# Kernel optimization log

Hardware: AMD Instinct MI355X
Metric: run time of the kernel (lower is better)

## Reference

```python
import jax, jax.numpy as jnp
import numpy as np

B, C, HH, WW, HEADS = 4, 64, 256, 256, 8
CH = C // HEADS              # 8 per-head dim
HID = int(C * 2.66)          # 170
EPS_LN = 1e-5
EPS = 1e-6
QK_NORM = 1.0
# crpe windows for 8 heads: {3:2, 5:3, 7:3}; each conv input split = head_split*Ch*2
WINDOWS = [(3, 2), (5, 3), (7, 3)]


def conv2d(x, w, b=None, groups=1, pad=0):
    out = jax.lax.conv_general_dilated(
        x, w, (1, 1), [(pad, pad), (pad, pad)],
        dimension_numbers=('NCHW', 'OIHW', 'NCHW'), feature_group_count=groups)
    return out if b is None else out + b[None, :, None, None]


def setup_inputs() -> dict:
    key = jax.random.key(0)
    ks = jax.random.split(key, 32)
    p = lambda k, shp, s=0.05: jax.random.normal(k, shp, jnp.float32) * s
    inp = {
        'x': jax.random.normal(ks[0], (B, HH * WW, C), jnp.float32),
        'ln1_w': jnp.ones((C,), jnp.float32) + p(ks[1], (C,), 0.01),
        'sca_w': p(ks[2], (C, C, 1, 1)), 'sca_b': p(ks[3], (C,)),
        'dw1_w': p(ks[4], (2 * C, C, 1, 1)),          # 1x1 dim->2dim
        'dw2_w': p(ks[5], (C, 2, 3, 3)),              # grouped 3x3, groups=C, in/grp=2
        'qkv_w': p(ks[6], (3 * C, C, 1, 1)),
        'qkv_dw_w': p(ks[7], (3 * C, 1, 3, 3)),       # depthwise 3x3
        'temperature': jnp.ones((HEADS, 1, 1), jnp.float32),
        'r3_w': p(ks[8], (2, 2 * CH, 3, 3)), 'r3_b': p(ks[9], (2,)),
        'r5_w': p(ks[10], (3, 2 * CH, 5, 5)), 'r5_b': p(ks[11], (3,)),
        'r7_w': p(ks[12], (3, 2 * CH, 7, 7)), 'r7_b': p(ks[13], (3,)),
        'proj_w': p(ks[14], (C, C, 1, 1)),
        'ln2_w': jnp.ones((C,), jnp.float32) + p(ks[15], (C,), 0.01),
        'pin_w': p(ks[16], (2 * HID, C, 1, 1)),
        'ffn_dw_w': p(ks[17], (2 * HID, 1, 3, 3)),
        'pout_w': p(ks[18], (C, HID, 1, 1)),
        'H': HH, 'W': WW,
    }
    return inp


def biasfree_ln(x, w):
    # BiasFree LayerNorm over channel dim of NCHW (var only, no mean-subtract)
    sigma = jnp.var(x, axis=1, keepdims=True)
    return x / jnp.sqrt(sigma + EPS_LN) * w[None, :, None, None]


def refine_att(q, k, H, W, convs):
    # q: (B,h,N,Ch)  k: (B,h,Ch,N) -> per-head conv relative position map (B,h,N,1)
    b, h, N, Ch = q.shape
    q_img = q.transpose(0, 1, 3, 2).reshape(b, h, Ch, H, W)
    k_img = k.reshape(b, h, Ch, H, W)
    qk = jnp.concatenate([q_img, k_img], axis=2).reshape(b, h * 2 * Ch, H, W)
    splits = np.cumsum([s * 2 * Ch for _, s in WINDOWS])[:-1]
    parts = jnp.split(qk, splits, axis=1)
    outs = [conv2d(xp, wt, bs, groups=g, pad=win // 2)
            for (win, g), (wt, bs), xp in zip(WINDOWS, convs, parts)]
    att = jnp.concatenate(outs, axis=1)           # (b, h, H, W)
    return att.reshape(b, h, 1, H * W).transpose(0, 1, 3, 2)  # (b,h,N,1)


def attention(x, sca_w, sca_b, dw1_w, dw2_w, qkv_w, qkv_dw_w, temperature,
              refine_convs, proj_w, H, W):
    b, c, _, _ = x.shape
    N = H * W
    xsca = conv2d(jnp.mean(x, axis=(2, 3), keepdims=True), sca_w, sca_b)
    x1 = conv2d(conv2d(x, dw1_w), dw2_w, groups=c, pad=1)
    qkv = conv2d(conv2d(x, qkv_w), qkv_dw_w, groups=3 * c, pad=1)
    q, k, v = jnp.split(qkv, 3, axis=1)
    q = q.reshape(b, HEADS, CH, N).transpose(0, 1, 3, 2)  # b h N Ch
    k = k.reshape(b, HEADS, CH, N)                        # b h Ch N
    v = v.reshape(b, HEADS, CH, N).transpose(0, 1, 3, 2)  # b h N Ch
    q = q / (jnp.linalg.norm(q, axis=-1, keepdims=True) / QK_NORM + EPS)
    k = k / (jnp.linalg.norm(k, axis=-2, keepdims=True) / QK_NORM + EPS)
    refine_w = jax.nn.sigmoid(refine_att(q, k, H, W, refine_convs))
    attn = k @ v                                           # b h Ch Ch
    out_num = jnp.sum(v, axis=-2, keepdims=True) + q @ attn
    ksum = jnp.sum(k, axis=-1, keepdims=True)              # b h Ch 1
    out_den = jnp.asarray(N, q.dtype) + q @ ksum + EPS     # b h N 1 (bcast to Ch)
    out = out_num / out_den * temperature
    out = out * refine_w
    out = out.transpose(0, 1, 3, 2).reshape(b, c, H, W)
    out = out * xsca * jax.nn.gelu(x1, approximate=False)
    return conv2d(out, proj_w)


def feedforward(x, pin_w, ffn_dw_w, pout_w):
    h = conv2d(x, pin_w)
    h = conv2d(h, ffn_dw_w, groups=2 * HID, pad=1)
    h1, h2 = jnp.split(h, 2, axis=1)
    return conv2d(jax.nn.gelu(h1, approximate=False) * h2, pout_w)


def reference(x, ln1_w, sca_w, sca_b, dw1_w, dw2_w, qkv_w, qkv_dw_w, temperature,
              r3_w, r3_b, r5_w, r5_b, r7_w, r7_b, proj_w, ln2_w,
              pin_w, ffn_dw_w, pout_w, H, W):
    b = x.shape[0]
    xi = x.reshape(b, H, W, C).transpose(0, 3, 1, 2)  # NCHW
    refine_convs = [(r3_w, r3_b), (r5_w, r5_b), (r7_w, r7_b)]
    xi = xi + attention(biasfree_ln(xi, ln1_w), sca_w, sca_b, dw1_w, dw2_w,
                        qkv_w, qkv_dw_w, temperature, refine_convs, proj_w, H, W)
    xi = xi + feedforward(biasfree_ln(xi, ln2_w), pin_w, ffn_dw_w, pout_w)
    return xi
```

## Files before the change

kernel.cpp:

```cpp
#include <hip/hip_runtime.h>
#include <math.h>
#include <stdio.h>

#define BB 4
#define NP 65536

typedef unsigned short u16;
typedef unsigned int u32;
typedef __attribute__((ext_vector_type(8))) short short8;
typedef __attribute__((ext_vector_type(4))) float f32x4;

__device__ __forceinline__ float bf2f(u16 u) { return __uint_as_float((u32)u << 16); }
__device__ __forceinline__ u16 f2bf(float f) {
  u32 u = __float_as_uint(f);
  u = (u + 0x7FFFu + ((u >> 16) & 1u)) >> 16;
  return (u16)u;
}
__device__ __forceinline__ float gelu_f(float x) {
  return 0.5f * x * (1.f + erff(x * 0.70710678118654752f));
}

__global__ __launch_bounds__(256) void k_trans_stats(const float* __restrict__ x,
                                                     float* __restrict__ xi,
                                                     u16* __restrict__ xb1,
                                                     float* __restrict__ meanraw) {
  __shared__ float tile[64 * 65];
  __shared__ float s1a[64], s2a[64], sig[64], cm[64];
  int b = blockIdx.y;
  long n0 = (long)blockIdx.x * 64;
  int t = threadIdx.x;
  for (int i = t; i < 4096; i += 256) {
    int nl = i >> 6, c = i & 63;
    tile[nl * 65 + c] = x[((long)b * NP + n0 + nl) * 64 + c];
  }
  if (t < 64) { s1a[t] = 0.f; s2a[t] = 0.f; cm[t] = 0.f; }
  __syncthreads();
  {
    int nl = t & 63, part = t >> 6;
    float p1 = 0.f, p2 = 0.f;
    for (int cc = 0; cc < 16; cc++) {
      float v = tile[nl * 65 + part * 16 + cc];
      p1 += v; p2 += v * v;
    }
    atomicAdd(&s1a[nl], p1); atomicAdd(&s2a[nl], p2);
  }
  __syncthreads();
  if (t < 64) {
    float m = s1a[t] * (1.f / 64.f);
    float var = s2a[t] * (1.f / 64.f) - m * m;
    sig[t] = rsqrtf(var + 1e-5f);
  }
  __syncthreads();
  int nl = t & 63;
  int part = t >> 6;
  float sgv = sig[nl];
  for (int j = 0; j < 16; j++) {
    int i = t + 256 * j;
    int c = i >> 6;
    float v = tile[nl * 65 + c];
    xi[((long)b * 64 + c) * NP + n0 + nl] = v;
    float a = v * sgv;
    for (int off = 32; off; off >>= 1) a += __shfl_down(a, off);
    if ((t & 63) == 0) atomicAdd(&cm[c], a);
  }
  {
    u16* rp = xb1 + ((long)b * NP + n0 + nl) * 64 + part * 16;
    uint4 pk[2];
    u32 tmp[8];
#pragma unroll
    for (int g = 0; g < 2; g++) {
#pragma unroll
      for (int e = 0; e < 4; e++) {
        float v0 = tile[nl * 65 + part * 16 + g * 8 + 2 * e] * sgv;
        float v1 = tile[nl * 65 + part * 16 + g * 8 + 2 * e + 1] * sgv;
        tmp[e] = (u32)f2bf(v0) | ((u32)f2bf(v1) << 16);
      }
      pk[g].x = tmp[0]; pk[g].y = tmp[1]; pk[g].z = tmp[2]; pk[g].w = tmp[3];
      *(uint4*)(rp + g * 8) = pk[g];
    }
  }
  __syncthreads();
  if (t < 64) atomicAdd(&meanraw[b * 64 + t], cm[t]);
}

__global__ void k_xsca(const float* __restrict__ meanraw, const float* __restrict__ lnw,
                       const float* __restrict__ sca_w, const float* __restrict__ sca_b,
                       float* __restrict__ xsca) {
  int t = threadIdx.x;
  int b = t >> 6, co = t & 63;
  float a = sca_b[co];
  for (int ci = 0; ci < 64; ci++)
    a += sca_w[co * 64 + ci] * meanraw[b * 64 + ci] * lnw[ci] * (1.f / 65536.f);
  xsca[t] = a;
}

__global__ void k_foldW1b(const float* __restrict__ qkv_w, const float* __restrict__ dw1_w,
                          const float* __restrict__ lnw, u16* __restrict__ W1b) {
  int i = blockIdx.x * 256 + threadIdx.x;
  if (i < 320 * 64) {
    int co = i >> 6, ci = i & 63;
    float w = (co < 192) ? qkv_w[co * 64 + ci] : dw1_w[(co - 192) * 64 + ci];
    W1b[i] = f2bf(w * lnw[ci]);
  }
}
__global__ void k_foldW2b(const float* __restrict__ pin_w, const float* __restrict__ lnw,
                          u16* __restrict__ W2b) {
  int i = blockIdx.x * 256 + threadIdx.x;
  if (i < 384 * 64) {
    int co = i >> 6, ci = i & 63;
    float v = 0.f;
    if (co < 340) {
      int pair = co >> 1, which = co & 1;
      v = pin_w[(pair + which * 170) * 64 + ci] * lnw[ci];
    }
    W2b[i] = f2bf(v);
  }
}
__global__ void k_foldWpb(const float* __restrict__ w, u16* __restrict__ Wpb) {
  int i = blockIdx.x * 256 + threadIdx.x;
  if (i < 4096) Wpb[i] = f2bf(w[i]);
}
__global__ void k_tpout(const float* __restrict__ w, float* __restrict__ WoT) {
  int i = blockIdx.x * 256 + threadIdx.x;
  if (i < 170 * 64) { int ci = i >> 6, co = i & 63; WoT[ci * 64 + co] = w[co * 170 + ci]; }
}

template <int EPI>
__global__ __launch_bounds__(256) void k_mgemm(const u16* __restrict__ in, long in_bs,
                                               const u16* __restrict__ W,
                                               u16* __restrict__ outp, long out_bs,
                                               float* __restrict__ xo,
                                               u16* __restrict__ xb2r) {
  int t = threadIdx.x;
  int lane = t & 63, wv = t >> 6;
  int l15 = lane & 15, quad = lane >> 4;
  int pxw = blockIdx.x * 256 + wv * 64;
  int co0 = blockIdx.y * 64;
  int b = blockIdx.z;
  const u16* inb = in + (long)b * in_bs;

  short8 aw[4][2];
#pragma unroll
  for (int t4 = 0; t4 < 4; t4++)
#pragma unroll
    for (int kf = 0; kf < 2; kf++)
      aw[t4][kf] = *(const short8*)(W + (long)(co0 + t4 * 16 + l15) * 64 + kf * 32 + quad * 8);

  f32x4 acc[4][4];
#pragma unroll
  for (int t4 = 0; t4 < 4; t4++)
#pragma unroll
    for (int p = 0; p < 4; p++) acc[t4][p] = (f32x4){0.f, 0.f, 0.f, 0.f};

#pragma unroll
  for (int p = 0; p < 4; p++) {
    long px = pxw + p * 16 + l15;
    short8 bf0 = *(const short8*)(inb + px * 64 + quad * 8);
    short8 bf1 = *(const short8*)(inb + px * 64 + 32 + quad * 8);
#pragma unroll
    for (int t4 = 0; t4 < 4; t4++) {
      acc[t4][p] = __builtin_amdgcn_mfma_f32_16x16x32_bf16(aw[t4][0], bf0, acc[t4][p], 0, 0, 0);
      acc[t4][p] = __builtin_amdgcn_mfma_f32_16x16x32_bf16(aw[t4][1], bf1, acc[t4][p], 0, 0, 0);
    }
  }

  if (EPI == 0) {
    u16* ob = outp + (long)b * out_bs;
#pragma unroll
    for (int t4 = 0; t4 < 4; t4++)
#pragma unroll
      for (int p = 0; p < 4; p++) {
#pragma unroll
        for (int reg = 0; reg < 4; reg++) {
          int co = co0 + t4 * 16 + quad * 4 + reg;
          ob[(long)co * NP + pxw + p * 16 + l15] = f2bf(acc[t4][p][reg]);
        }
      }
  } else {
#pragma unroll
    for (int p = 0; p < 4; p++) {
      long px = pxw + p * 16 + l15;
      float xv[16];
      float s1 = 0.f, s2 = 0.f;
#pragma unroll
      for (int t4 = 0; t4 < 4; t4++)
#pragma unroll
        for (int reg = 0; reg < 4; reg++) {
          int co = t4 * 16 + quad * 4 + reg;
          float v = xo[((long)b * 64 + co) * NP + px] + acc[t4][p][reg];
          xv[t4 * 4 + reg] = v;
          s1 += v; s2 += v * v;
        }
      s1 += __shfl_xor(s1, 16); s2 += __shfl_xor(s2, 16);
      s1 += __shfl_xor(s1, 32); s2 += __shfl_xor(s2, 32);
      float m = s1 * (1.f / 64.f);
      float var = s2 * (1.f / 64.f) - m * m;
      float sg = rsqrtf(var + 1e-5f);
#pragma unroll
      for (int t4 = 0; t4 < 4; t4++)
#pragma unroll
        for (int reg = 0; reg < 4; reg++) {
          int co = t4 * 16 + quad * 4 + reg;
          xo[((long)b * 64 + co) * NP + px] = xv[t4 * 4 + reg];
        }
      u16* rp = xb2r + ((long)b * NP + px) * 64;
#pragma unroll
      for (int t4 = 0; t4 < 4; t4++) {
        u32 u0 = (u32)f2bf(xv[t4 * 4 + 0] * sg) | ((u32)f2bf(xv[t4 * 4 + 1] * sg) << 16);
        u32 u1 = (u32)f2bf(xv[t4 * 4 + 2] * sg) | ((u32)f2bf(xv[t4 * 4 + 3] * sg) << 16);
        uint2 pk; pk.x = u0; pk.y = u1;
        *(uint2*)(rp + t4 * 16 + quad * 4) = pk;
      }
    }
  }
}

__device__ __forceinline__ void dw4(const u16* __restrict__ img, int y, int x0, int lane,
                                    const float* __restrict__ w9, float d[4]) {
  d[0] = 0.f; d[1] = 0.f; d[2] = 0.f; d[3] = 0.f;
#pragma unroll
  for (int dy = -1; dy <= 1; dy++) {
    int r = y + dy;
    float v1, v2, v3, v4;
    if ((unsigned)r < 256u) {
      ushort4 u = *(const ushort4*)(img + r * 256 + x0);
      v1 = bf2f(u.x); v2 = bf2f(u.y); v3 = bf2f(u.z); v4 = bf2f(u.w);
    } else { v1 = 0.f; v2 = 0.f; v3 = 0.f; v4 = 0.f; }
    float v0 = __shfl_up(v4, 1);  if (lane == 0)  v0 = 0.f;
    float v5 = __shfl_down(v1, 1); if (lane == 63) v5 = 0.f;
    float w0 = w9[(dy + 1) * 3], w1 = w9[(dy + 1) * 3 + 1], w2 = w9[(dy + 1) * 3 + 2];
    d[0] += w0 * v0 + w1 * v1 + w2 * v2;
    d[1] += w0 * v1 + w1 * v2 + w2 * v3;
    d[2] += w0 * v2 + w1 * v3 + w2 * v4;
    d[3] += w0 * v3 + w1 * v4 + w2 * v5;
  }
}

__global__ __launch_bounds__(256) void k_dwqkv(const u16* __restrict__ P,
                                               const float* __restrict__ dww,
                                               u16* __restrict__ Qn, u16* __restrict__ Kn,
                                               u16* __restrict__ Vn) {
  int t = threadIdx.x;
  int lane = t & 63, wv = t >> 6;
  int by = blockIdx.y;
  int ph = by >> 3, h = by & 7;
  int b = blockIdx.z;
  int y = blockIdx.x * 4 + wv;
  int x0 = lane * 4;
  long n = (long)y * 256 + x0;
  int cbase = ph * 64 + h * 8;
  const u16* Pb = P + ((long)b * 192 + cbase) * NP;
  const float* wb = dww + cbase * 9;

  float v[8][4];
#pragma unroll
  for (int c = 0; c < 8; c++)
    dw4(Pb + (long)c * NP, y, x0, lane, wb + c * 9, v[c]);

  if (ph < 2) {
    float s2[4] = {0.f, 0.f, 0.f, 0.f};
#pragma unroll
    for (int c = 0; c < 8; c++)
#pragma unroll
      for (int j = 0; j < 4; j++) s2[j] += v[c][j] * v[c][j];
#pragma unroll
    for (int j = 0; j < 4; j++) s2[j] = 1.f / (sqrtf(s2[j]) + 1e-6f);
#pragma unroll
    for (int c = 0; c < 8; c++)
#pragma unroll
      for (int j = 0; j < 4; j++) v[c][j] *= s2[j];
  }
  u16* dst = (ph == 0) ? Qn : (ph == 1) ? Kn : Vn;
#pragma unroll
  for (int c = 0; c < 8; c++) {
    ushort4 st;
    st.x = f2bf(v[c][0]); st.y = f2bf(v[c][1]);
    st.z = f2bf(v[c][2]); st.w = f2bf(v[c][3]);
    *(ushort4*)(dst + ((long)b * 64 + h * 8 + c) * NP + n) = st;
  }
}

__global__ __launch_bounds__(256) void k_stats(const u16* __restrict__ Kn,
                                               const u16* __restrict__ Vn,
                                               float* __restrict__ stats) {
  int t = threadIdx.x;
  int lane = t & 63;
  int h = blockIdx.y, b = blockIdx.z;
  long px = (long)blockIdx.x * 1024 + t * 4;
  const u16* Kb = Kn + ((long)b * 64 + h * 8) * NP + px;
  const u16* Vb = Vn + ((long)b * 64 + h * 8) * NP + px;
  float kf[8][4], vf[8][4];
#pragma unroll
  for (int c = 0; c < 8; c++) {
    ushort4 ku = *(const ushort4*)(Kb + (long)c * NP);
    kf[c][0] = bf2f(ku.x); kf[c][1] = bf2f(ku.y);
    kf[c][2] = bf2f(ku.z); kf[c][3] = bf2f(ku.w);
  }
#pragma unroll
  for (int c = 0; c < 8; c++) {
    ushort4 vu = *(const ushort4*)(Vb + (long)c * NP);
    vf[c][0] = bf2f(vu.x); vf[c][1] = bf2f(vu.y);
    vf[c][2] = bf2f(vu.z); vf[c][3] = bf2f(vu.w);
  }
  __shared__ float sred[80];
  if (t < 80) sred[t] = 0.f;
  __syncthreads();
#pragma unroll
  for (int i = 0; i < 8; i++) {
#pragma unroll
    for (int j = 0; j < 8; j++) {
      float a = kf[i][0] * vf[j][0] + kf[i][1] * vf[j][1] +
                kf[i][2] * vf[j][2] + kf[i][3] * vf[j][3];
      a += __shfl_xor(a, 1); a += __shfl_xor(a, 2); a += __shfl_xor(a, 4);
      a += __shfl_xor(a, 8); a += __shfl_xor(a, 16); a += __shfl_xor(a, 32);
      if (lane == ((i * 8 + j) & 63)) atomicAdd(&sred[i * 8 + j], a);
    }
    {
      float a = kf[i][0] + kf[i][1] + kf[i][2] + kf[i][3];
      a += __shfl_xor(a, 1); a += __shfl_xor(a, 2); a += __shfl_xor(a, 4);
      a += __shfl_xor(a, 8); a += __shfl_xor(a, 16); a += __shfl_xor(a, 32);
      if (lane == ((64 + i) & 63)) atomicAdd(&sred[64 + i], a);
    }
    {
      float a = vf[i][0] + vf[i][1] + vf[i][2] + vf[i][3];
      a += __shfl_xor(a, 1); a += __shfl_xor(a, 2); a += __shfl_xor(a, 4);
      a += __shfl_xor(a, 8); a += __shfl_xor(a, 16); a += __shfl_xor(a, 32);
      if (lane == ((72 + i) & 63)) atomicAdd(&sred[72 + i], a);
    }
  }
  __syncthreads();
  if (t < 80) atomicAdd(&stats[((long)b * 8 + h) * 80 + t], sred[t]);
}

__global__ __launch_bounds__(256) void k_dwg(const u16* __restrict__ P,
                                             const float* __restrict__ dw2_w,
                                             u16* __restrict__ G) {
  int t = threadIdx.x;
  int lane = t & 63, wv = t >> 6;
  int c = blockIdx.y, b = blockIdx.z;
  int y = blockIdx.x * 4 + wv;
  int x0 = lane * 4;
  long n = (long)y * 256 + x0;
  const u16* Pb = P + (long)b * 128 * NP;
  float d1[4], d2[4];
  dw4(Pb + (long)(2 * c) * NP, y, x0, lane, dw2_w + c * 18, d1);
  dw4(Pb + (long)(2 * c + 1) * NP, y, x0, lane, dw2_w + c * 18 + 9, d2);
  ushort4 st;
  st.x = f2bf(gelu_f(d1[0] + d2[0])); st.y = f2bf(gelu_f(d1[1] + d2[1]));
  st.z = f2bf(gelu_f(d1[2] + d2[2])); st.w = f2bf(gelu_f(d1[3] + d2[3]));
  *(ushort4*)(G + ((long)b * 64 + c) * NP + n) = st;
}

__global__ __launch_bounds__(256) void k_dwgate(const u16* __restrict__ P,
                                                const float* __restrict__ dww,
                                                u16* __restrict__ Hb) {
  int t = threadIdx.x;
  int lane = t & 63, wv = t >> 6;
  int c = blockIdx.y, b = blockIdx.z;
  int y = blockIdx.x * 4 + wv;
  int x0 = lane * 4;
  long n = (long)y * 256 + x0;
  const u16* Pb = P + (long)b * 384 * NP;
  float d1[4], d2[4];
  dw4(Pb + (long)(2 * c) * NP, y, x0, lane, dww + c * 9, d1);
  dw4(Pb + (long)(2 * c + 1) * NP, y, x0, lane, dww + (170 + c) * 9, d2);
  ushort4 st;
  st.x = f2bf(gelu_f(d1[0]) * d2[0]); st.y = f2bf(gelu_f(d1[1]) * d2[1]);
  st.z = f2bf(gelu_f(d1[2]) * d2[2]); st.w = f2bf(gelu_f(d1[3]) * d2[3]);
  *(ushort4*)(Hb + ((long)b * 170 + c) * NP + n) = st;
}

__device__ __forceinline__ float bfe_elem(uint2 v, int e) {
  u32 w = (e < 2) ? v.x : v.y;
  return bf2f((e & 1) ? (u16)(w >> 16) : (u16)w);
}

template <int WIN>
__device__ __forceinline__ void dwacc(const u16* __restrict__ img, int y, int x0, int lane,
                                      const float* __restrict__ w, float a[4]) {
  const int R = WIN / 2;
#pragma unroll
  for (int dy = -R; dy <= R; dy++) {
    int r = y + dy;
    uint2 q; q.x = 0u; q.y = 0u;
    if ((unsigned)r < 256u) q = *(const uint2*)(img + r * 256 + x0);
    uint2 ql, qr;
    ql.x = (u32)__shfl_up((int)q.x, 1);  ql.y = (u32)__shfl_up((int)q.y, 1);
    qr.x = (u32)__shfl_down((int)q.x, 1); qr.y = (u32)__shfl_down((int)q.y, 1);
    if (lane == 0)  { ql.x = 0u; ql.y = 0u; }
    if (lane == 63) { qr.x = 0u; qr.y = 0u; }
    float f[4 + 2 * R];
#pragma unroll
    for (int i = 0; i < R; i++) f[i] = bfe_elem(ql, 4 - R + i);
    f[R + 0] = bf2f((u16)q.x); f[R + 1] = bf2f((u16)(q.x >> 16));
    f[R + 2] = bf2f((u16)q.y); f[R + 3] = bf2f((u16)(q.y >> 16));
#pragma unroll
    for (int i = 0; i < R; i++) f[R + 4 + i] = bfe_elem(qr, i);
    const float* wr = w + (dy + R) * WIN;
#pragma unroll
    for (int dx = 0; dx < WIN; dx++) {
      float wv = wr[dx];
      a[0] += wv * f[dx];     a[1] += wv * f[dx + 1];
      a[2] += wv * f[dx + 2]; a[3] += wv * f[dx + 3];
    }
  }
}

template <int WIN>
__device__ void refine_body(const u16* __restrict__ Qh, const u16* __restrict__ Kh,
                            const float* __restrict__ wp, float bias,
                            float* __restrict__ ro, int y, int x0, int lane) {
  float a[4] = {bias, bias, bias, bias};
#pragma unroll
  for (int ph = 0; ph < 2; ph++) {
    const u16* src = ph ? Kh : Qh;
#pragma unroll 2
    for (int ch = 0; ch < 8; ch++)
      dwacc<WIN>(src + (long)ch * NP, y, x0, lane, wp + (ph * 8 + ch) * WIN * WIN, a);
  }
  float4 o;
  o.x = 1.f / (1.f + expf(-a[0])); o.y = 1.f / (1.f + expf(-a[1]));
  o.z = 1.f / (1.f + expf(-a[2])); o.w = 1.f / (1.f + expf(-a[3]));
  *(float4*)(ro + (long)y * 256 + x0) = o;
}

__global__ __launch_bounds__(256) void k_refine(
    const u16* __restrict__ Qn, const u16* __restrict__ Kn,
    const float* __restrict__ r3w, const float* __restrict__ r3b,
    const float* __restrict__ r5w, const float* __restrict__ r5b,
    const float* __restrict__ r7w, const float* __restrict__ r7b,
    float* __restrict__ refW) {
  int t = threadIdx.x, lane = t & 63, wv = t >> 6;
  int h = (blockIdx.y + 5) & 7;
  int b = blockIdx.z;
  int y = blockIdx.x * 4 + wv, x0 = lane * 4;
  const u16* Qh = Qn + ((long)b * 64 + h * 8) * NP;
  const u16* Kh = Kn + ((long)b * 64 + h * 8) * NP;
  float* ro = refW + ((long)(b * 8 + h)) * NP;
  if (h < 2)      refine_body<3>(Qh, Kh, r3w + h * 16 * 9, r3b[h], ro, y, x0, lane);
  else if (h < 5) refine_body<5>(Qh, Kh, r5w + (h - 2) * 16 * 25, r5b[h - 2], ro, y, x0, lane);
  else            refine_body<7>(Qh, Kh, r7w + (h - 5) * 16 * 49, r7b[h - 5], ro, y, x0, lane);
}

__global__ __launch_bounds__(256) void k_attn(
    const u16* __restrict__ Qn, const float* __restrict__ stats,
    const float* __restrict__ refw, const float* __restrict__ temp,
    const float* __restrict__ xsca, const u16* __restrict__ G,
    u16* __restrict__ Orows) {
  int b = blockIdx.y;
  int t = threadIdx.x;
  __shared__ float s[640];
  __shared__ float sx[64];
  for (int i = t; i < 640; i += 256) s[i] = stats[(long)b * 640 + i];
  if (t < 64) sx[t] = xsca[b * 64 + t];
  __syncthreads();
  long n = (long)blockIdx.x * 256 + t;
  u16* rp = Orows + ((long)b * NP + n) * 64;
#pragma unroll
  for (int h = 0; h < 8; h++) {
    const float* sh = s + h * 80;
    float q[8];
#pragma unroll
    for (int i = 0; i < 8; i++) q[i] = bf2f(Qn[((long)b * 64 + h * 8 + i) * NP + n]);
    float den = 65536.f + 1e-6f;
#pragma unroll
    for (int i = 0; i < 8; i++) den += q[i] * sh[64 + i];
    float tr = temp[h] * refw[((long)b * 8 + h) * NP + n] / den;
    u32 pk[4];
#pragma unroll
    for (int j2 = 0; j2 < 4; j2++) {
      float o01[2];
#pragma unroll
      for (int e = 0; e < 2; e++) {
        int j = j2 * 2 + e;
        float num = sh[72 + j];
#pragma unroll
        for (int i = 0; i < 8; i++) num += q[i] * sh[i * 8 + j];
        int ci = h * 8 + j;
        o01[e] = num * tr * sx[ci] * bf2f(G[((long)b * 64 + ci) * NP + n]);
      }
      pk[j2] = (u32)f2bf(o01[0]) | ((u32)f2bf(o01[1]) << 16);
    }
    uint4 v; v.x = pk[0]; v.y = pk[1]; v.z = pk[2]; v.w = pk[3];
    *(uint4*)(rp + h * 8) = v;
  }
}

__global__ __launch_bounds__(256) void k_pout(const u16* __restrict__ Hb,
                                              const float* __restrict__ WoT,
                                              float* __restrict__ xo) {
  int n = blockIdx.x * 256 + threadIdx.x;
  int b = blockIdx.z;
  const u16* ip = Hb + (long)b * 170 * NP + n;
  float acc[64];
#pragma unroll
  for (int j = 0; j < 64; j++) acc[j] = 0.f;
#pragma unroll 2
  for (int ci = 0; ci < 170; ci++) {
    float xv = bf2f(ip[(long)ci * NP]);
    const float* wr = WoT + ci * 64;
#pragma unroll
    for (int j = 0; j < 64; j++) acc[j] += wr[j] * xv;
  }
  float* xp = xo + (long)b * 64 * NP + n;
#pragma unroll
  for (int c = 0; c < 64; c++) xp[(long)c * NP] += acc[c];
}

extern "C" void kernel_launch(void* const* d_in, const int* in_sizes, int n_in,
                              void* d_out, int out_size, void* d_ws, size_t ws_size,
                              hipStream_t stream) {
  const float* x        = (const float*)d_in[0];
  const float* ln1_w    = (const float*)d_in[1];
  const float* sca_w    = (const float*)d_in[2];
  const float* sca_b    = (const float*)d_in[3];
  const float* dw1_w    = (const float*)d_in[4];
  const float* dw2_w    = (const float*)d_in[5];
  const float* qkv_w    = (const float*)d_in[6];
  const float* qkv_dw_w = (const float*)d_in[7];
  const float* temp     = (const float*)d_in[8];
  const float* r3w = (const float*)d_in[9],  *r3b = (const float*)d_in[10];
  const float* r5w = (const float*)d_in[11], *r5b = (const float*)d_in[12];
  const float* r7w = (const float*)d_in[13], *r7b = (const float*)d_in[14];
  const float* proj_w   = (const float*)d_in[15];
  const float* ln2_w    = (const float*)d_in[16];
  const float* pin_w    = (const float*)d_in[17];
  const float* ffn_dw_w = (const float*)d_in[18];
  const float* pout_w   = (const float*)d_in[19];
  float* out = (float*)d_out;
  char* wsb = (char*)d_ws;

  const size_t Mi = 1048576;
  u16* xb1   = (u16*)(wsb);
  u16* Qn    = (u16*)(wsb + 32 * Mi);
  u16* Kn    = (u16*)(wsb + 64 * Mi);
  u16* G     = (u16*)(wsb + 96 * Mi);
  u16* Preg  = (u16*)(wsb + 128 * Mi);
  float* refW    = (float*)(wsb + 224 * Mi);
  float* Fm      = (float*)(wsb + 232 * Mi);
  float* stats   = Fm;
  float* meanraw = Fm + 2560;
  float* xscab   = Fm + 2816;
  float* WoT     = Fm + 3072;
  u16* W1b = (u16*)(Fm + 13952);
  u16* W2b = W1b + 20480;
  u16* Wpb = W2b + 24576;
  u16* xb2 = xb1;
  u16* Orows = Kn;
  u16* Hb = Qn;
  u16* Vn = G;

  const size_t needed = 232 * Mi + 13952 * 4 + (20480 + 24576 + 4096) * 2;
  if (ws_size < needed) {
    fprintf(stderr, "kernel_launch: ws_size %zu < needed %zu\n", ws_size, needed);
    return;
  }

  hipMemsetAsync(stats, 0, (2560 + 256) * 4, stream);
  k_foldW1b<<<80, 256, 0, stream>>>(qkv_w, dw1_w, ln1_w, W1b);
  k_foldW2b<<<96, 256, 0, stream>>>(pin_w, ln2_w, W2b);
  k_foldWpb<<<16, 256, 0, stream>>>(proj_w, Wpb);
  k_tpout<<<43, 256, 0, stream>>>(pout_w, WoT);

  k_trans_stats<<<dim3(1024, BB), 256, 0, stream>>>(x, out, xb1, meanraw);
  k_xsca<<<1, 256, 0, stream>>>(meanraw, ln1_w, sca_w, sca_b, xscab);

  k_mgemm<0><<<dim3(256, 3, BB), 256, 0, stream>>>(xb1, (long)NP * 64, W1b,
                                                   Preg, 192L * NP, nullptr, nullptr);
  k_dwqkv<<<dim3(64, 24, BB), 256, 0, stream>>>(Preg, qkv_dw_w, Qn, Kn, Vn);
  k_stats<<<dim3(64, 8, BB), 256, 0, stream>>>(Kn, Vn, stats);

  k_mgemm<0><<<dim3(256, 2, BB), 256, 0, stream>>>(xb1, (long)NP * 64, W1b + 192 * 64,
                                                   Preg, 128L * NP, nullptr, nullptr);
  k_dwg<<<dim3(64, 64, BB), 256, 0, stream>>>(Preg, dw2_w, G);

  k_refine<<<dim3(64, 8, BB), 256, 0, stream>>>(Qn, Kn, r3w, r3b, r5w, r5b, r7w, r7b, refW);
  k_attn<<<dim3(256, BB), 256, 0, stream>>>(Qn, stats, refW, temp, xscab, G, Orows);

  k_mgemm<1><<<dim3(256, 1, BB), 256, 0, stream>>>(Orows, (long)NP * 64, Wpb,
                                                   nullptr, 0, out, xb2);

  for (int pass = 0; pass < 2; pass++) {
    k_mgemm<0><<<dim3(256, 6, 2), 256, 0, stream>>>(xb2 + (long)pass * 2 * NP * 64,
                                                    (long)NP * 64, W2b,
                                                    Preg, 384L * NP, nullptr, nullptr);
    k_dwgate<<<dim3(64, 170, 2), 256, 0, stream>>>(Preg, ffn_dw_w,
                                                   Hb + (long)pass * 2 * 170 * NP);
  }
  k_pout<<<dim3(256, 1, BB), 256, 0, stream>>>(Hb, WoT, out);
}
```

Measured before the change: 859.7 us.

## Rewrite FFN output projection as bf16 MFMA GEMM with LDS-transposed tiles

The final pointwise projection (170->64 channels) previously ran as a scalar fp32 loop, with each thread keeping 64 accumulators and reading weights from global memory. It now stages a 64-pixel by 192-channel bf16 tile in shared memory, transposed to pixel-major with padding, and runs 16x16x32 bf16 MFMA instructions against a zero-padded bf16 weight matrix. This swaps register-heavy scalar FMAs for matrix-core work and raises the block count. In exchange, weights are rounded to bf16, the tile loads are strided 2-byte gathers, and the output stores are scattered.

```diff
diff --git a/kernel.cpp b/kernel.cpp
--- a/kernel.cpp
+++ b/kernel.cpp
@@ -120,9 +120,12 @@
   int i = blockIdx.x * 256 + threadIdx.x;
   if (i < 4096) Wpb[i] = f2bf(w[i]);
 }
-__global__ void k_tpout(const float* __restrict__ w, float* __restrict__ WoT) {
+__global__ void k_tpoutb(const float* __restrict__ w, u16* __restrict__ Wob) {
   int i = blockIdx.x * 256 + threadIdx.x;
-  if (i < 170 * 64) { int ci = i >> 6, co = i & 63; WoT[ci * 64 + co] = w[co * 170 + ci]; }
+  if (i < 64 * 192) {
+    int co = i / 192, ci = i - co * 192;
+    Wob[i] = (ci < 170) ? f2bf(w[co * 170 + ci]) : (u16)0;
+  }
 }
 
 template <int EPI>
@@ -487,24 +490,55 @@
 }
 
 __global__ __launch_bounds__(256) void k_pout(const u16* __restrict__ Hb,
-                                              const float* __restrict__ WoT,
+                                              const u16* __restrict__ Wob,
                                               float* __restrict__ xo) {
-  int n = blockIdx.x * 256 + threadIdx.x;
+  __shared__ u16 tile[64 * 196];
+  int t = threadIdx.x;
+  int lane = t & 63, wv = t >> 6;
+  int l15 = lane & 15, quad = lane >> 4;
   int b = blockIdx.z;
-  const u16* ip = Hb + (long)b * 170 * NP + n;
-  float acc[64];
-#pragma unroll
-  for (int j = 0; j < 64; j++) acc[j] = 0.f;
-#pragma unroll 2
-  for (int ci = 0; ci < 170; ci++) {
-    float xv = bf2f(ip[(long)ci * NP]);
-    const float* wr = WoT + ci * 64;
-#pragma unroll
-    for (int j = 0; j < 64; j++) acc[j] += wr[j] * xv;
-  }
-  float* xp = xo + (long)b * 64 * NP + n;
-#pragma unroll
-  for (int c = 0; c < 64; c++) xp[(long)c * NP] += acc[c];
+  int px0 = blockIdx.x * 64;
+  const u16* ib = Hb + (long)b * 170 * NP + px0;
+#pragma unroll
+  for (int i = 0; i < 12; i++) {
+    int task = t + i * 256;
+    int q = task >> 6, px = task & 63;
+    int ci0 = q * 4;
+    u32 w0 = 0u, w1 = 0u;
+    if (ci0 < 170)     w0 = (u32)ib[(long)ci0 * NP + px];
+    if (ci0 + 1 < 170) w0 |= ((u32)ib[(long)(ci0 + 1) * NP + px]) << 16;
+    if (ci0 + 2 < 170) w1 = (u32)ib[(long)(ci0 + 2) * NP + px];
+    if (ci0 + 3 < 170) w1 |= ((u32)ib[(long)(ci0 + 3) * NP + px]) << 16;
+    uint2 pk; pk.x = w0; pk.y = w1;
+    *(uint2*)(tile + px * 196 + ci0) = pk;
+  }
+  __syncthreads();
+
+  f32x4 acc[4];
+#pragma unroll
+  for (int t4 = 0; t4 < 4; t4++) acc[t4] = (f32x4){0.f, 0.f, 0.f, 0.f};
+  const u16* tb = tile + (wv * 16 + l15) * 196;
+#pragma unroll
+  for (int kf = 0; kf < 6; kf++) {
+    union { uint2 u2[2]; short8 s8; } cv;
+    cv.u2[0] = *(const uint2*)(tb + kf * 32 + quad * 8);
+    cv.u2[1] = *(const uint2*)(tb + kf * 32 + quad * 8 + 4);
+    short8 bfr = cv.s8;
+#pragma unroll
+    for (int t4 = 0; t4 < 4; t4++) {
+      short8 aw = *(const short8*)(Wob + (long)(t4 * 16 + l15) * 192 + kf * 32 + quad * 8);
+      acc[t4] = __builtin_amdgcn_mfma_f32_16x16x32_bf16(aw, bfr, acc[t4], 0, 0, 0);
+    }
+  }
+  long pxg = px0 + wv * 16 + l15;
+  float* xb = xo + (long)b * 64 * NP;
+#pragma unroll
+  for (int t4 = 0; t4 < 4; t4++)
+#pragma unroll
+    for (int reg = 0; reg < 4; reg++) {
+      int co = t4 * 16 + quad * 4 + reg;
+      xb[(long)co * NP + pxg] += acc[t4][reg];
+    }
 }
 
 extern "C" void kernel_launch(void* const* d_in, const int* in_sizes, int n_in,
@@ -541,7 +575,7 @@
   float* stats   = Fm;
   float* meanraw = Fm + 2560;
   float* xscab   = Fm + 2816;
-  float* WoT     = Fm + 3072;
+  u16* Wob       = (u16*)(Fm + 3072);
   u16* W1b = (u16*)(Fm + 13952);
   u16* W2b = W1b + 20480;
   u16* Wpb = W2b + 24576;
@@ -560,7 +594,7 @@
   k_foldW1b<<<80, 256, 0, stream>>>(qkv_w, dw1_w, ln1_w, W1b);
   k_foldW2b<<<96, 256, 0, stream>>>(pin_w, ln2_w, W2b);
   k_foldWpb<<<16, 256, 0, stream>>>(proj_w, Wpb);
-  k_tpout<<<43, 256, 0, stream>>>(pout_w, WoT);
+  k_tpoutb<<<48, 256, 0, stream>>>(pout_w, Wob);
 
   k_trans_stats<<<dim3(1024, BB), 256, 0, stream>>>(x, out, xb1, meanraw);
   k_xsca<<<1, 256, 0, stream>>>(meanraw, ln1_w, sca_w, sca_b, xscab);
@@ -587,5 +621,5 @@
     k_dwgate<<<dim3(64, 170, 2), 256, 0, stream>>>(Preg, ffn_dw_w,
                                                    Hb + (long)pass * 2 * 170 * NP);
   }
-  k_pout<<<dim3(256, 1, BB), 256, 0, stream>>>(Hb, WoT, out);
-}
+  k_pout<<<dim3(1024, 1, BB), 256, 0, stream>>>(Hb, Wob, out);
+}
```

After: 854.9 us. About the same (-0.6%).
